# Performance work log

Measured on AMD Instinct MI355X. Metric: run time of the kernel, lower is better.

Reference implementation:

```python
import jax, jax.numpy as jnp
import numpy as np

HEADS = 4
NBLK = 4
UPS = 4
EPS = 1e-5


def conv3x3(x, w, b):
    # x: NCHW, w: OIHW (3x3, stride 1, pad 1 -> SAME)
    y = jax.lax.conv_general_dilated(x, w, (1, 1), 'SAME',
                                     dimension_numbers=('NCHW', 'OIHW', 'NCHW'))
    return y + b[None, :, None, None]


def layer_norm(x, g, b):
    mu = jnp.mean(x, axis=-1, keepdims=True)
    var = jnp.var(x, axis=-1, keepdims=True)
    return (x - mu) * jax.lax.rsqrt(var + EPS) * g + b


def attention(x, wq, bq, wp, bp):
    # NOTE: the torch module's reshape flattens all windows into one sequence,
    # so this is mathematically global attention over all H*W tokens.
    B, H, W, C = x.shape
    L = H * W
    hd = C // HEADS
    t = x.reshape(B, L, C)
    qkv = (t @ wq + bq).reshape(B, L, 3, HEADS, hd).transpose(2, 0, 3, 1, 4)
    q, k, v = qkv[0], qkv[1], qkv[2]                      # (B, nh, L, hd)
    attn = jax.nn.softmax(jnp.einsum('bnld,bnmd->bnlm', q, k) * (hd ** -0.5), axis=-1)
    o = jnp.einsum('bnlm,bnmd->bnld', attn, v)            # (B, nh, L, hd)
    o = o.transpose(0, 2, 1, 3).reshape(B, L, C)
    return (o @ wp + bp).reshape(B, H, W, C)


def swin_block(x, g1, b1, wq, bq, wp, bp, g2, b2, w1, bf1, w2, bf2):
    shortcut = x
    h = jnp.transpose(x, (0, 2, 3, 1))                    # NHWC
    h = layer_norm(h, g1, b1)
    h = attention(h, wq, bq, wp, bp) + h
    h = layer_norm(h, g2, b2)
    h = (jax.nn.gelu(h @ w1 + bf1, approximate=False) @ w2 + bf2) + h
    return shortcut + jnp.transpose(h, (0, 3, 1, 2))


def pixel_shuffle(x, r):
    B, C, H, W = x.shape
    c = C // (r * r)
    x = x.reshape(B, c, r, r, H, W).transpose(0, 1, 4, 2, 5, 3)
    return x.reshape(B, c, H * r, W * r)


def setup_inputs() -> dict:
    key = jax.random.key(0)
    ks = jax.random.split(key, 16)
    d = 48

    def rn(k, shape, s=0.02):
        return jax.random.normal(k, shape, jnp.float32) * s

    return {
        'x': jax.random.normal(ks[0], (2, 3, 64, 64), jnp.float32),
        'conv_first_w': rn(ks[1], (d, 3, 3, 3)),
        'conv_first_b': jnp.zeros((d,), jnp.float32),
        'norm1_g': jnp.ones((NBLK, d), jnp.float32),
        'norm1_b': jnp.zeros((NBLK, d), jnp.float32),
        'qkv_w': rn(ks[2], (NBLK, d, 3 * d)),
        'qkv_b': jnp.zeros((NBLK, 3 * d), jnp.float32),
        'proj_w': rn(ks[3], (NBLK, d, d)),
        'proj_b': jnp.zeros((NBLK, d), jnp.float32),
        'norm2_g': jnp.ones((NBLK, d), jnp.float32),
        'norm2_b': jnp.zeros((NBLK, d), jnp.float32),
        'fc1_w': rn(ks[4], (NBLK, d, 2 * d)),
        'fc1_b': jnp.zeros((NBLK, 2 * d), jnp.float32),
        'fc2_w': rn(ks[5], (NBLK, 2 * d, d)),
        'fc2_b': jnp.zeros((NBLK, d), jnp.float32),
        'up_w': rn(ks[6], (d * UPS * UPS, d, 3, 3)),
        'up_b': jnp.zeros((d * UPS * UPS,), jnp.float32),
        'last_w': rn(ks[7], (3, d, 3, 3)),
        'last_b': jnp.zeros((3,), jnp.float32),
    }


def reference(x, conv_first_w, conv_first_b, norm1_g, norm1_b, qkv_w, qkv_b,
              proj_w, proj_b, norm2_g, norm2_b, fc1_w, fc1_b, fc2_w, fc2_b,
              up_w, up_b, last_w, last_b):
    h = conv3x3(x, conv_first_w, conv_first_b)
    for i in range(NBLK):
        h = swin_block(h, norm1_g[i], norm1_b[i], qkv_w[i], qkv_b[i],
                       proj_w[i], proj_b[i], norm2_g[i], norm2_b[i],
                       fc1_w[i], fc1_b[i], fc2_w[i], fc2_b[i])
    h = conv3x3(h, up_w, up_b)
    h = pixel_shuffle(h, UPS)
    return conv3x3(h, last_w, last_b)
```

## Files before the change

kernel.cpp:

```cpp
#include <hip/hip_runtime.h>
#include <hip/hip_bf16.h>
#include <math.h>

#define BB 2
#define D 48
#define HH 64
#define WW 64
#define LL 4096
#define NHEADS 4
#define HD 12
#define NBLK 4
#define CUP 768
#define H2 256
#define W2 256

#define NSPLIT 4
#define OPART_STRIDE 393216

typedef __attribute__((ext_vector_type(8))) short short8v;
typedef __attribute__((ext_vector_type(4))) float f32x4;
typedef unsigned long long u64;

__device__ __forceinline__ short f2bf(float f) {
    __hip_bfloat16 h = __float2bfloat16(f);
    union { __hip_bfloat16 b; short s; } u; u.b = h; return u.s;
}
__device__ __forceinline__ float bf2f(short s) {
    union { float f; unsigned u; } x;
    x.u = ((unsigned)(unsigned short)s) << 16;
    return x.f;
}
__device__ __forceinline__ float exp2_raw(float x) {
    float r; asm("v_exp_f32 %0, %1" : "=v"(r) : "v"(x)); return r;
}

__global__ void conv3x3_kernel(const float* __restrict__ in, const float* __restrict__ w,
                               const float* __restrict__ bias, float* __restrict__ out,
                               int Cin, int Cout) {
    int idx = blockIdx.x * blockDim.x + threadIdx.x;
    int total = BB * Cout * HH * WW;
    if (idx >= total) return;
    int x = idx % WW;
    int y = (idx / WW) % HH;
    int co = (idx / (WW * HH)) % Cout;
    int b = idx / (WW * HH * Cout);
    float s = bias[co];
    for (int ci = 0; ci < Cin; ci++) {
        const float* ip = in + ((size_t)(b * Cin + ci) * HH) * WW;
        const float* wp = w + (size_t)(co * Cin + ci) * 9;
        #pragma unroll
        for (int ky = 0; ky < 3; ky++) {
            int iy = y + ky - 1;
            if (iy < 0 || iy >= HH) continue;
            #pragma unroll
            for (int kx = 0; kx < 3; kx++) {
                int ix = x + kx - 1;
                if (ix < 0 || ix >= WW) continue;
                s += ip[iy * WW + ix] * wp[ky * 3 + kx];
            }
        }
    }
    out[idx] = s;
}

__global__ __launch_bounds__(256) void pack_h_kernel(const float* __restrict__ h,
                                                     short* __restrict__ hbfp) {
    int idx = blockIdx.x * 256 + threadIdx.x;
    const int TOT = 2 * 66 * 66 * 48;
    if (idx >= TOT + 64) return;
    if (idx >= TOT) { hbfp[idx] = 0; return; }
    int ci = idx % 48;
    int p = idx / 48;
    int xx = p % 66;
    int q = p / 66;
    int yy = q % 66;
    int b = q / 66;
    short v = 0;
    if (yy >= 1 && yy <= 64 && xx >= 1 && xx <= 64)
        v = f2bf(h[((size_t)(b * 48 + ci) << 12) + (yy - 1) * 64 + (xx - 1)]);
    hbfp[idx] = v;
}

__global__ __launch_bounds__(256) void pack_w_kernel(const float* __restrict__ w,
                                                     short* __restrict__ Wp) {
    int idx = blockIdx.x * 256 + threadIdx.x;
    if (idx >= 48 * 14 * 512) return;
    int j = idx & 7;
    int g = (idx >> 3) & 3;
    int col = (idx >> 5) & 15;
    int s = (idx >> 9) % 14;
    int n16 = idx / (14 * 512);
    int k = 32 * s + 8 * g + j;
    short v = 0;
    if (k < 432) {
        int tap = k / 48, ci = k - tap * 48;
        int co = n16 * 16 + col;
        v = f2bf(w[((size_t)co * 48 + ci) * 9 + tap]);
    }
    Wp[idx] = v;
}

__global__ __launch_bounds__(256) void pack_lw_kernel(const float* __restrict__ w,
                                                      short* __restrict__ Wp2) {
    int idx = blockIdx.x * 256 + threadIdx.x;
    if (idx >= 14 * 512) return;
    int j = idx & 7;
    int g = (idx >> 3) & 3;
    int col = (idx >> 5) & 15;
    int s = idx >> 9;
    int k = 32 * s + 8 * g + j;
    short v = 0;
    if (k < 432 && col < 3) {
        int tap = k / 48, ci = k - tap * 48;
        v = f2bf(w[((size_t)col * 48 + ci) * 9 + tap]);
    }
    Wp2[idx] = v;
}

__global__ __launch_bounds__(256) void conv_up_mfma_kernel(const short* __restrict__ hbfp,
                                                           const short* __restrict__ Wp,
                                                           const float* __restrict__ bias,
                                                           short* __restrict__ U) {
    int tid = threadIdx.x;
    int wave = tid >> 6, lane = tid & 63;
    int t = blockIdx.x * 4 + wave;
    int mt = t / 48;
    int n16 = t - mt * 48;
    int b = mt >> 8;
    int rem = mt & 255;
    int y = rem >> 2;
    int xt = rem & 3;
    int col = lane & 15;
    int g = lane >> 4;
    int x = xt * 16 + col;

    const short* Bp = Wp + (size_t)n16 * (14 * 512) + col * 32 + g * 8;
    const short* zb = hbfp + 2 * 66 * 66 * 48;

    f32x4 acc = {0.f, 0.f, 0.f, 0.f};
    #pragma unroll
    for (int s = 0; s < 14; s++) {
        int gg = 4 * s + g;
        int tap = (gg * 171) >> 10;
        int cig = gg - tap * 6;
        int dy = (tap * 11) >> 5;
        int dx = tap - dy * 3;
        const short* ap = hbfp + ((size_t)((b * 66 + y + dy) * 66 + (x + dx)) * 48 + cig * 8);
        ap = (gg < 54) ? ap : zb;
        short8v av = *(const short8v*)ap;
        short8v bv = *(const short8v*)(Bp + s * 512);
        acc = __builtin_amdgcn_mfma_f32_16x16x32_bf16(av, bv, acc, 0, 0, 0);
    }

    int co = n16 * 16 + col;
    float bval = bias[co];
    int ic = co >> 4, dyq = (co >> 2) & 3, dxq = co & 3;
    int y2 = 4 * y + dyq;
    short* Ur = U + ((size_t)(b * 256 + y2) * 256) * 48 + ic;
    #pragma unroll
    for (int j = 0; j < 4; j++) {
        int r = 4 * g + j;
        int x2 = 4 * (xt * 16 + r) + dxq;
        Ur[(size_t)x2 * 48] = f2bf(acc[j] + bval);
    }
}

__global__ void zero16_kernel(u64* __restrict__ p, int n) {
    int i = blockIdx.x * 256 + threadIdx.x;
    if (i >= n) return;
    u64 fill = 0ull;
    int rel = 8 * i - 2097152;
    if (rel >= 0 && rel < 524288 && (((rel >> 5) & 15) == 12))
        fill = 0x3F803F803F803F80ull;
    p[2 * i] = fill;
    p[2 * i + 1] = fill;
}

__global__ __launch_bounds__(256) void fused_ln1_qkv_kernel(
    const float* __restrict__ hsrc, const float* __restrict__ g1, const float* __restrict__ b1,
    const float* __restrict__ w, const float* __restrict__ bias,
    float* __restrict__ ln1, short* __restrict__ Qbf, short* __restrict__ Kbf,
    short* __restrict__ Vr) {
    __shared__ float hs[48 * 17];
    __shared__ float lnr[16 * 49];
    __shared__ float wl[48 * 144];
    int blk = blockIdx.x;
    int b = blk >> 8;
    int pos0 = (blk & 255) * 16;
    int tid = threadIdx.x;

    for (int i = tid; i < 48 * 144; i += 256) wl[i] = w[i];
    for (int i = tid; i < 48 * 16; i += 256) {
        int ch = i >> 4, p = i & 15;
        hs[ch * 17 + p] = hsrc[((size_t)b * 48 + ch) * 4096 + pos0 + p];
    }
    __syncthreads();

    int tok = tid >> 4, oct = tid & 15;
    int pos = pos0 + tok;
    float v[3];
    float s = 0.f, s2 = 0.f;
    #pragma unroll
    for (int j = 0; j < 3; j++) {
        float x = hs[(oct * 3 + j) * 17 + tok];
        v[j] = x; s += x; s2 += x * x;
    }
    #pragma unroll
    for (int msk = 1; msk < 16; msk <<= 1) {
        s += __shfl_xor(s, msk, 64);
        s2 += __shfl_xor(s2, msk, 64);
    }
    float mu = s * (1.f / 48.f);
    float var = s2 * (1.f / 48.f) - mu * mu;
    float rs = rsqrtf(var + 1e-5f);
    float* go = ln1 + ((size_t)b * 4096 + pos) * 48 + oct * 3;
    #pragma unroll
    for (int j = 0; j < 3; j++) {
        int c = oct * 3 + j;
        float y = (v[j] - mu) * rs * g1[c] + b1[c];
        lnr[tok * 49 + c] = y;
        go[j] = y;
    }
    __syncthreads();

    int c0 = oct * 9;
    float acc[9];
    #pragma unroll
    for (int j = 0; j < 9; j++) acc[j] = bias[c0 + j];
    #pragma unroll 4
    for (int k = 0; k < 48; k++) {
        float a = lnr[tok * 49 + k];
        const float* wr = wl + k * 144 + c0;
        #pragma unroll
        for (int j = 0; j < 9; j++) acc[j] += a * wr[j];
    }

    const float scale = 0.41647023f;
    int sstep = pos >> 5, r = pos & 31;
    int g2 = (r < 16) ? (r >> 2) : ((r - 16) >> 2);
    int j2 = (r < 16) ? (r & 3) : 4 + ((r - 16) & 3);
    #pragma unroll
    for (int j = 0; j < 9; j++) {
        int c = c0 + j;
        int which = (c >= 96) ? 2 : (c >= 48 ? 1 : 0);
        int rem = c - which * 48;
        int hh = rem / 12;
        int dd = rem - hh * 12;
        int bh = b * 4 + hh;
        if (which == 0)
            Qbf[((size_t)bh * 4096 + pos) * 32 + dd] = f2bf(acc[j] * scale);
        else if (which == 1)
            Kbf[((size_t)bh * 4096 + pos) * 32 + dd] = f2bf(acc[j]);
        else
            Vr[((size_t)bh * 128 + sstep) * 512 + dd * 32 + g2 * 8 + j2] = f2bf(acc[j]);
    }
}

__global__ __launch_bounds__(256) void fused_mlp_kernel(
    const float* __restrict__ opart, const float* __restrict__ ssump,
    const float* __restrict__ pwg, const float* __restrict__ pb,
    const float* __restrict__ ln1, const float* __restrict__ g2v, const float* __restrict__ b2v,
    const float* __restrict__ f1w, const float* __restrict__ f1b,
    const float* __restrict__ f2w, const float* __restrict__ f2b,
    float* __restrict__ hbuf) {
    __shared__ float sm[14640];
    float* wp  = sm;
    float* w1  = sm + 2304;
    float* w2  = sm + 6912;
    float* arf = sm + 11520;
    float* lnr = sm + 12304;
    float* m1v = sm + 13088;

    int blk = blockIdx.x;
    int b = blk >> 8;
    int pos0 = (blk & 255) * 16;
    int tid = threadIdx.x;

    for (int i = tid; i < 2304; i += 256) wp[i] = pwg[i];
    for (int i = tid; i < 4608; i += 256) w1[i] = f1w[i];
    for (int i = tid; i < 4608; i += 256) w2[i] = f2w[i];
    for (int i = tid; i < 768; i += 256) {
        int t = i / 48, c = i - (i / 48) * 48;
        int hh = c / 12;
        size_t base = ((size_t)b * 4096 + pos0) * 48 + i;
        float stot = 0.f, s = 0.f;
        #pragma unroll
        for (int sp = 0; sp < NSPLIT; sp++) {
            stot += ssump[((size_t)sp * 8 + b * 4 + hh) * 4096 + pos0 + t];
            s += opart[base + (size_t)sp * OPART_STRIDE];
        }
        arf[t * 49 + c] = s / stot;
    }
    __syncthreads();

    int tok = tid >> 4, oct = tid & 15;
    size_t gtok = (size_t)b * 4096 + pos0 + tok;
    int c0 = oct * 3;
    float acc[3];
    #pragma unroll
    for (int j = 0; j < 3; j++) acc[j] = pb[c0 + j];
    #pragma unroll 4
    for (int k = 0; k < 48; k++) {
        float a = arf[tok * 49 + k];
        const float* wr = wp + k * 48 + c0;
        #pragma unroll
        for (int j = 0; j < 3; j++) acc[j] += a * wr[j];
    }
    const float* rp = ln1 + gtok * 48 + c0;
    float x[3]; float s = 0.f, s2 = 0.f;
    #pragma unroll
    for (int j = 0; j < 3; j++) {
        float t = acc[j] + rp[j];
        x[j] = t; s += t; s2 += t * t;
    }
    #pragma unroll
    for (int msk = 1; msk < 16; msk <<= 1) {
        s += __shfl_xor(s, msk, 64);
        s2 += __shfl_xor(s2, msk, 64);
    }
    float mu = s * (1.f / 48.f), var = s2 * (1.f / 48.f) - mu * mu;
    float rs = rsqrtf(var + 1e-5f);
    #pragma unroll
    for (int j = 0; j < 3; j++) {
        int c = c0 + j;
        lnr[tok * 49 + c] = (x[j] - mu) * rs * g2v[c] + b2v[c];
    }
    __syncthreads();

    int d0 = oct * 6;
    float a2[6];
    #pragma unroll
    for (int j = 0; j < 6; j++) a2[j] = f1b[d0 + j];
    #pragma unroll 4
    for (int k = 0; k < 48; k++) {
        float a = lnr[tok * 49 + k];
        const float* wr = w1 + k * 96 + d0;
        #pragma unroll
        for (int j = 0; j < 6; j++) a2[j] += a * wr[j];
    }
    #pragma unroll
    for (int j = 0; j < 6; j++) {
        float g = a2[j];
        m1v[tok * 97 + d0 + j] = 0.5f * g * (1.f + erff(g * 0.70710678118654752f));
    }
    __syncthreads();

    float f2acc[3];
    #pragma unroll
    for (int j = 0; j < 3; j++) f2acc[j] = f2b[c0 + j];
    #pragma unroll 4
    for (int k = 0; k < 96; k++) {
        float a = m1v[tok * 97 + k];
        const float* wr = w2 + k * 48 + c0;
        #pragma unroll
        for (int j = 0; j < 3; j++) f2acc[j] += a * wr[j];
    }
    __syncthreads();
    #pragma unroll
    for (int j = 0; j < 3; j++)
        arf[tok * 49 + c0 + j] = f2acc[j] + lnr[tok * 49 + c0 + j];
    __syncthreads();

    for (int i = tid; i < 768; i += 256) {
        int c = i >> 4, t = i & 15;
        hbuf[(((size_t)(b * 48 + c)) << 12) + pos0 + t] += arf[t * 49 + c];
    }
}

#define LOADCH(P, c) { \
    _Pragma("unroll") \
    for (int s_ = 0; s_ < 4; s_++) { \
        const short* kp_ = Kb + ((size_t)((c) * 128 + s_ * 32 + col)) * 32 + g * 8; \
        P##k0[s_] = *(const short8v*)(kp_); \
        P##k1[s_] = *(const short8v*)(kp_ + 512); \
        P##v[s_]  = *(const short8v*)(Vrb + ((c) * 4 + s_) * 512 + vbase); \
    } }

#define STEP2(kc0, kc1, vv) { \
    f32x4 z_ = {0.f, 0.f, 0.f, 0.f}; \
    f32x4 sa1 = __builtin_amdgcn_mfma_f32_16x16x32_bf16(kc0, qb0, z_, 0, 0, 0); \
    f32x4 sa2 = __builtin_amdgcn_mfma_f32_16x16x32_bf16(kc1, qb0, z_, 0, 0, 0); \
    f32x4 sb1 = __builtin_amdgcn_mfma_f32_16x16x32_bf16(kc0, qb1, z_, 0, 0, 0); \
    f32x4 sb2 = __builtin_amdgcn_mfma_f32_16x16x32_bf16(kc1, qb1, z_, 0, 0, 0); \
    float a0 = exp2_raw(sa1[0]), a1 = exp2_raw(sa1[1]); \
    float a2 = exp2_raw(sa1[2]), a3 = exp2_raw(sa1[3]); \
    float a4 = exp2_raw(sa2[0]), a5 = exp2_raw(sa2[1]); \
    float a6 = exp2_raw(sa2[2]), a7 = exp2_raw(sa2[3]); \
    float e0 = exp2_raw(sb1[0]), e1 = exp2_raw(sb1[1]); \
    float e2 = exp2_raw(sb1[2]), e3 = exp2_raw(sb1[3]); \
    float e4 = exp2_raw(sb2[0]), e5 = exp2_raw(sb2[1]); \
    float e6 = exp2_raw(sb2[2]), e7 = exp2_raw(sb2[3]); \
    union { short8v sv; unsigned u[4]; } pa_, pe_; \
    asm("v_cvt_pk_bf16_f32 %0, %1, %2" : "=v"(pa_.u[0]) : "v"(a0), "v"(a1)); \
    asm("v_cvt_pk_bf16_f32 %0, %1, %2" : "=v"(pa_.u[1]) : "v"(a2), "v"(a3)); \
    asm("v_cvt_pk_bf16_f32 %0, %1, %2" : "=v"(pa_.u[2]) : "v"(a4), "v"(a5)); \
    asm("v_cvt_pk_bf16_f32 %0, %1, %2" : "=v"(pa_.u[3]) : "v"(a6), "v"(a7)); \
    asm("v_cvt_pk_bf16_f32 %0, %1, %2" : "=v"(pe_.u[0]) : "v"(e0), "v"(e1)); \
    asm("v_cvt_pk_bf16_f32 %0, %1, %2" : "=v"(pe_.u[1]) : "v"(e2), "v"(e3)); \
    asm("v_cvt_pk_bf16_f32 %0, %1, %2" : "=v"(pe_.u[2]) : "v"(e4), "v"(e5)); \
    asm("v_cvt_pk_bf16_f32 %0, %1, %2" : "=v"(pe_.u[3]) : "v"(e6), "v"(e7)); \
    o0 = __builtin_amdgcn_mfma_f32_16x16x32_bf16(vv, pa_.sv, o0, 0, 0, 0); \
    o1 = __builtin_amdgcn_mfma_f32_16x16x32_bf16(vv, pe_.sv, o1, 0, 0, 0); }

#define COMPUTECH2(P) { \
    STEP2(P##k0[0], P##k1[0], P##v[0]); \
    STEP2(P##k0[1], P##k1[1], P##v[1]); \
    STEP2(P##k0[2], P##k1[2], P##v[2]); \
    STEP2(P##k0[3], P##k1[3], P##v[3]); }

__global__ __launch_bounds__(256) void attn_mfma_kernel(const short* __restrict__ Qbf,
                                                        const short* __restrict__ Kbf,
                                                        const short* __restrict__ Vr,
                                                        float* __restrict__ opart,
                                                        float* __restrict__ ssump) {
    int bid = blockIdx.x;
    int bh = bid & 7;
    int qblk = (bid >> 3) & 31;
    int split = bid >> 8;
    int h = bh & 3, b = bh >> 2;
    int tid = threadIdx.x;
    int wave = tid >> 6;
    int lane = tid & 63;
    int q0 = qblk * 128 + wave * 32;
    int col = lane & 15;
    int g = lane >> 4;

    const short* Kb  = Kbf + (size_t)bh * LL * 32 + (size_t)split * 1024 * 32;
    const short* Vrb = Vr + (size_t)bh * 65536 + (size_t)split * 32 * 512;
    int vbase = col * 32 + g * 8;

    short8v qb0 = *(const short8v*)(Qbf + ((size_t)bh * LL + q0 + col) * 32 + g * 8);
    short8v qb1 = *(const short8v*)(Qbf + ((size_t)bh * LL + q0 + 16 + col) * 32 + g * 8);

    f32x4 o0 = {0.f, 0.f, 0.f, 0.f};
    f32x4 o1 = {0.f, 0.f, 0.f, 0.f};

    short8v a_k0[4], a_k1[4], a_v[4];
    short8v b_k0[4], b_k1[4], b_v[4];

    LOADCH(a_, 0);
    for (int c = 0; c < 8; c += 2) {
        LOADCH(b_, c + 1);
        COMPUTECH2(a_);
        if (c + 2 < 8) LOADCH(a_, c + 2);
        COMPUTECH2(b_);
    }

    float ssa = __shfl(o0[0], 48 + col, 64);
    float ssb = __shfl(o1[0], 48 + col, 64);

    float* op = opart + (size_t)split * OPART_STRIDE
              + ((size_t)b * 4096 + q0 + col) * 48 + h * HD;
    #pragma unroll
    for (int j = 0; j < 4; j++) {
        int d = 4 * g + j;
        if (d < HD) {
            op[d] = o0[j];
            op[16 * 48 + d] = o1[j];
        }
    }
    if (lane < 16) {
        float* sp = ssump + ((size_t)split * 8 + bh) * 4096 + q0 + col;
        sp[0] = ssa;
        sp[16] = ssb;
    }
}

__global__ __launch_bounds__(256) void lastconv_mfma_kernel(const short* __restrict__ U,
                                                            const short* __restrict__ Wp2,
                                                            const short* __restrict__ zb,
                                                            const float* __restrict__ bias,
                                                            float* __restrict__ out) {
    int tid = threadIdx.x;
    int wave = tid >> 6, lane = tid & 63;
    int t = blockIdx.x * 4 + wave;
    int xt = t & 15;
    int yy = (t >> 4) & 255;
    int b = t >> 12;
    int col = lane & 15, g = lane >> 4;
    int x = xt * 16 + col;

    const short* Ub = U + (size_t)b * 65536 * 48;
    const short* Bp = Wp2 + col * 32 + g * 8;

    f32x4 acc = {0.f, 0.f, 0.f, 0.f};
    #pragma unroll
    for (int s = 0; s < 14; s++) {
        int gg = 4 * s + g;
        int tap = (gg * 171) >> 10;
        int cig = gg - tap * 6;
        int dy3 = (tap * 11) >> 5;
        int dy = dy3 - 1;
        int dx = tap - dy3 * 3 - 1;
        int yq = yy + dy, xq = x + dx;
        bool ok = (gg < 54) && (yq >= 0) && (yq < 256) && (xq >= 0) && (xq < 256);
        const short* ap = Ub + (ptrdiff_t)(yq * 256 + xq) * 48 + cig * 8;
        ap = ok ? ap : zb;
        short8v av = *(const short8v*)ap;
        short8v bv = *(const short8v*)(Bp + s * 512);
        acc = __builtin_amdgcn_mfma_f32_16x16x32_bf16(av, bv, acc, 0, 0, 0);
    }

    if (col < 3) {
        float bval = bias[col];
        float* op = out + ((size_t)(b * 3 + col) * 256 + yy) * 256 + xt * 16 + 4 * g;
        #pragma unroll
        for (int j = 0; j < 4; j++)
            op[j] = acc[j] + bval;
    }
}

static inline int gs(int n) { return (n + 255) / 256; }

extern "C" void kernel_launch(void* const* d_in, const int* in_sizes, int n_in,
                              void* d_out, int out_size, void* d_ws, size_t ws_size,
                              hipStream_t stream) {
    const float* x    = (const float*)d_in[0];
    const float* cf_w = (const float*)d_in[1];
    const float* cf_b = (const float*)d_in[2];
    const float* n1g  = (const float*)d_in[3];
    const float* n1b  = (const float*)d_in[4];
    const float* qkvw = (const float*)d_in[5];
    const float* qkvb = (const float*)d_in[6];
    const float* pw   = (const float*)d_in[7];
    const float* pb   = (const float*)d_in[8];
    const float* n2g  = (const float*)d_in[9];
    const float* n2b  = (const float*)d_in[10];
    const float* f1w  = (const float*)d_in[11];
    const float* f1b  = (const float*)d_in[12];
    const float* f2w  = (const float*)d_in[13];
    const float* f2b  = (const float*)d_in[14];
    const float* upw  = (const float*)d_in[15];
    const float* upb  = (const float*)d_in[16];
    const float* lw   = (const float*)d_in[17];
    const float* lb   = (const float*)d_in[18];

    float* ws = (float*)d_ws;
    const int S_h = BB * D * LL;
    float* A_h   = ws;
    float* pool  = ws + S_h;
    float* A_ln1 = pool;

    short* U_bf = (short*)pool;
    float* o_part = pool + 1572864;
    short* Qbf  = (short*)(pool + 3538944);
    short* Kbf  = Qbf + BB * NHEADS * LL * 32;
    short* Vr   = Kbf + BB * NHEADS * LL * 32;
    short* hbfp = (short*)(pool + 4849664);
    short* Wp   = (short*)(pool + 5058784);
    short* Wp2  = (short*)(pool + 5230816);
    float* ssum_part = pool + 5898240;

    conv3x3_kernel<<<gs(S_h), 256, 0, stream>>>(x, cf_w, cf_b, A_h, 3, D);

    zero16_kernel<<<1536, 256, 0, stream>>>((u64*)Qbf, 393216);
    pack_w_kernel<<<1344, 256, 0, stream>>>(upw, Wp);
    pack_lw_kernel<<<28, 256, 0, stream>>>(lw, Wp2);

    for (int i = 0; i < NBLK; i++) {
        fused_ln1_qkv_kernel<<<512, 256, 0, stream>>>(
            A_h, n1g + i * D, n1b + i * D,
            qkvw + (size_t)i * D * 3 * D, qkvb + i * 3 * D,
            A_ln1, Qbf, Kbf, Vr);
        attn_mfma_kernel<<<8 * 32 * NSPLIT, 256, 0, stream>>>(Qbf, Kbf, Vr, o_part, ssum_part);
        fused_mlp_kernel<<<512, 256, 0, stream>>>(
            o_part, ssum_part, pw + (size_t)i * D * D, pb + i * D,
            A_ln1, n2g + i * D, n2b + i * D,
            f1w + (size_t)i * D * 2 * D, f1b + i * 2 * D,
            f2w + (size_t)i * 2 * D * D, f2b + i * D,
            A_h);
    }

    pack_h_kernel<<<1634, 256, 0, stream>>>(A_h, hbfp);
    conv_up_mfma_kernel<<<6144, 256, 0, stream>>>(hbfp, Wp, upb, U_bf);

    lastconv_mfma_kernel<<<2048, 256, 0, stream>>>(
        U_bf, Wp2, hbfp + 2 * 66 * 66 * 48, lb, (float*)d_out);
}
```

Baseline: 310.0 us.

## Reuse activation fragments across all output tiles in up-conv and stage writes in LDS

The upsampling conv kernel now has each wave keep its 14 A-fragments in registers and loop over all 48 output-channel tiles, double-buffering the weight fragment loads. Before, every wave recomputed the A loads for one tile. Results are staged in shared memory so the pixel-shuffled output can be written as contiguous 16-byte rows instead of scattered 2-byte stores. The cost is a much smaller grid (256 blocks of 128 threads), which lowers parallelism and occupancy on a large GPU, plus heavy register pressure from holding three arrays of 14 fragments.

After: 293.1 us. 1.06x faster.

```diff
diff --git a/kernel.cpp b/kernel.cpp
--- a/kernel.cpp
+++ b/kernel.cpp
@@ -117,15 +117,29 @@
     Wp2[idx] = v;
 }
 
-__global__ __launch_bounds__(256) void conv_up_mfma_kernel(const short* __restrict__ hbfp,
+#define CU_LOADB(P, n) { \
+    _Pragma("unroll") \
+    for (int s_ = 0; s_ < 14; s_++) \
+        P[s_] = *(const short8v*)(Wb + (size_t)(n) * 7168 + s_ * 512); }
+
+#define CU_COMP(P, n) { \
+    f32x4 acc = {0.f, 0.f, 0.f, 0.f}; \
+    _Pragma("unroll") \
+    for (int s_ = 0; s_ < 14; s_++) \
+        acc = __builtin_amdgcn_mfma_f32_16x16x32_bf16(av[s_], P[s_], acc, 0, 0, 0); \
+    float bval = bias[(n) * 16 + col]; \
+    _Pragma("unroll") \
+    for (int j = 0; j < 4; j++) \
+        Sw[sbase + j * 192 + (n)] = f2bf(acc[j] + bval); }
+
+__global__ __launch_bounds__(128) void conv_up_mfma_kernel(const short* __restrict__ hbfp,
                                                            const short* __restrict__ Wp,
                                                            const float* __restrict__ bias,
                                                            short* __restrict__ U) {
+    __shared__ short Sb[2][12288];
     int tid = threadIdx.x;
     int wave = tid >> 6, lane = tid & 63;
-    int t = blockIdx.x * 4 + wave;
-    int mt = t / 48;
-    int n16 = t - mt * 48;
+    int mt = blockIdx.x * 2 + wave;
     int b = mt >> 8;
     int rem = mt & 255;
     int y = rem >> 2;
@@ -134,10 +148,9 @@
     int g = lane >> 4;
     int x = xt * 16 + col;
 
-    const short* Bp = Wp + (size_t)n16 * (14 * 512) + col * 32 + g * 8;
     const short* zb = hbfp + 2 * 66 * 66 * 48;
 
-    f32x4 acc = {0.f, 0.f, 0.f, 0.f};
+    short8v av[14];
     #pragma unroll
     for (int s = 0; s < 14; s++) {
         int gg = 4 * s + g;
@@ -147,21 +160,29 @@
         int dx = tap - dy * 3;
         const short* ap = hbfp + ((size_t)((b * 66 + y + dy) * 66 + (x + dx)) * 48 + cig * 8);
         ap = (gg < 54) ? ap : zb;
-        short8v av = *(const short8v*)ap;
-        short8v bv = *(const short8v*)(Bp + s * 512);
-        acc = __builtin_amdgcn_mfma_f32_16x16x32_bf16(av, bv, acc, 0, 0, 0);
-    }
-
-    int co = n16 * 16 + col;
-    float bval = bias[co];
-    int ic = co >> 4, dyq = (co >> 2) & 3, dxq = co & 3;
-    int y2 = 4 * y + dyq;
-    short* Ur = U + ((size_t)(b * 256 + y2) * 256) * 48 + ic;
-    #pragma unroll
-    for (int j = 0; j < 4; j++) {
-        int r = 4 * g + j;
-        int x2 = 4 * (xt * 16 + r) + dxq;
-        Ur[(size_t)x2 * 48] = f2bf(acc[j] + bval);
+        av[s] = *(const short8v*)ap;
+    }
+
+    const short* Wb = Wp + col * 32 + g * 8;
+    short* Sw = Sb[wave];
+    int dyq = col >> 2, dxq = col & 3;
+    int sbase = dyq * 3072 + (16 * g + dxq) * 48;
+
+    short8v Ba[14], Bb[14];
+    CU_LOADB(Ba, 0);
+    for (int n = 0; n < 48; n += 2) {
+        CU_LOADB(Bb, n + 1);
+        CU_COMP(Ba, n);
+        if (n + 2 < 48) CU_LOADB(Ba, n + 2);
+        CU_COMP(Bb, n + 1);
+    }
+
+    short* Ub = U + (((size_t)(b * 256 + 4 * y) * 256) + xt * 64) * 48;
+    for (int i = lane; i < 1536; i += 64) {
+        int row = i / 384;
+        int w8 = i - row * 384;
+        short8v v = *(const short8v*)(Sw + (size_t)i * 8);
+        *(short8v*)(Ub + (size_t)row * 256 * 48 + w8 * 8) = v;
     }
 }
 
@@ -572,7 +593,7 @@
     }
 
     pack_h_kernel<<<1634, 256, 0, stream>>>(A_h, hbfp);
-    conv_up_mfma_kernel<<<6144, 256, 0, stream>>>(hbfp, Wp, upb, U_bf);
+    conv_up_mfma_kernel<<<256, 128, 0, stream>>>(hbfp, Wp, upb, U_bf);
 
     lastconv_mfma_kernel<<<2048, 256, 0, stream>>>(
         U_bf, Wp2, hbfp + 2 * 66 * 66 * 48, lb, (float*)d_out);
```
